# Kernel optimization log

Measured on AMD Instinct MI355X. Metric: run time of the kernel, lower is better.

The kernel has to match this reference:

```python
import jax, jax.numpy as jnp
import numpy as np

N_NODES = 100000
N_EDGES = 1600000
DIM = 128
N_LAYERS = 3
N_GRAPHS = 2048


def setup_inputs() -> dict:
    key = jax.random.key(0)
    ks = jax.random.split(key, 6)
    x = jax.random.normal(ks[0], (N_NODES, DIM), dtype=jnp.float32)
    edge_index = jax.random.randint(ks[1], (2, N_EDGES), 0, N_NODES, dtype=jnp.int64)
    batch = jnp.sort(jax.random.randint(ks[2], (N_NODES,), 0, N_GRAPHS, dtype=jnp.int64))
    scale = 1.0 / np.sqrt(DIM)
    W1 = jax.random.normal(ks[3], (N_LAYERS, DIM, DIM), dtype=jnp.float32) * scale
    b1 = jnp.zeros((N_LAYERS, DIM), dtype=jnp.float32)
    W2 = jax.random.normal(ks[4], (N_LAYERS, DIM, DIM), dtype=jnp.float32) * scale
    b2 = jnp.zeros((N_LAYERS, DIM), dtype=jnp.float32)
    return {"x": x, "edge_index": edge_index, "batch": batch,
            "W1": W1, "b1": b1, "W2": W2, "b2": b2}


def reference(x, edge_index, batch, W1, b1, W2, b2):
    src, dst = edge_index[0], edge_index[1]
    n = x.shape[0]
    n_layers = W1.shape[0]
    for l in range(n_layers):
        # GINConv (eps=0): h_i = MLP( sum_{j in N(i)} x_j + x_i )
        agg = jax.ops.segment_sum(x[src], dst, num_segments=n)  # [N, D]
        h = agg + x
        h = jnp.maximum(h @ W1[l] + b1[l], 0.0) @ W2[l] + b2[l]
        x = jnp.maximum(h, 0.0)  # outer self.act
    # global_mean_pool over graph ids
    sums = jax.ops.segment_sum(x, batch, num_segments=N_GRAPHS)  # [G, D]
    counts = jax.ops.segment_sum(jnp.ones((n,), x.dtype), batch, num_segments=N_GRAPHS)
    return sums / jnp.maximum(counts, 1.0)[:, None]
```

## Files before the change

kernel.cpp:

```cpp
#include <hip/hip_runtime.h>
#include <hip/hip_bf16.h>
#include <stdint.h>

#define N_NODES  100000
#define N_PAD    100032
#define N_EDGES  1600000
#define DIM      128
#define N_LAYERS 3
#define N_GRAPHS 2048

#define BSHIFT   8
#define NBUCKET  391
#define P1CHUNK  4096
#define P1GRID   391

typedef _Float16 f16;
typedef __attribute__((ext_vector_type(4))) _Float16 f16x4;
typedef __attribute__((ext_vector_type(8))) _Float16 f16x8;
typedef __attribute__((ext_vector_type(4))) float f32x4;

#define MFMA16(a, b, c) __builtin_amdgcn_mfma_f32_16x16x32_f16((a), (b), (c), 0, 0, 0)

#define OFF_OFFS  0u
#define OFF_BHT   400064u
#define OFF_GCUR  401664u
#define OFF_BLKH  403264u
#define OFF_ESRC  1014848u
#define OFF_PAIR  7414848u
#define OFF_X16   13814848u
#define OFF_A16   39423040u
#define OFF_B16   65031232u
#define OFF_W1T   90639424u
#define OFF_W2T   90737728u


#define CVTX_BLOCKS 6250
#define CVTW_BLOCKS 384
#define ZERO_BLOCKS 128
#define PRE_GRID    (CVTX_BLOCKS + CVTW_BLOCKS + P1GRID + ZERO_BLOCKS)

__global__ __launch_bounds__(256) void k_pre(
    const float* __restrict__ x, const float* __restrict__ W1, const float* __restrict__ W2,
    f16* __restrict__ x16, f16* __restrict__ W1t, f16* __restrict__ W2t,
    const int* __restrict__ dst, int* __restrict__ btot, int* __restrict__ blkh,
    float* __restrict__ outp)
{
    __shared__ int h[NBUCKET];
    int b = blockIdx.x, tid = threadIdx.x;
    if (b < CVTX_BLOCKS) {
        size_t i = ((size_t)b * 256 + tid) * 8;
        float4 v0 = *(const float4*)&x[i];
        float4 v1 = *(const float4*)&x[i + 4];
        f16x8 o;
        o[0] = (f16)v0.x; o[1] = (f16)v0.y; o[2] = (f16)v0.z; o[3] = (f16)v0.w;
        o[4] = (f16)v1.x; o[5] = (f16)v1.y; o[6] = (f16)v1.z; o[7] = (f16)v1.w;
        *(f16x8*)&x16[i] = o;
    } else if (b < CVTX_BLOCKS + CVTW_BLOCKS) {
        int t = (b - CVTX_BLOCKS) * 256 + tid;
        bool first = t < 49152;
        const float* W = first ? W1 : W2;
        f16* Wt = first ? W1t : W2t;
        int u = first ? t : t - 49152;
        int l = u >> 14;
        int kn = u & 16383;
        int k = kn >> 7, nn = kn & 127;
        Wt[l * 16384 + nn * 128 + k] = (f16)W[u];
    } else if (b < CVTX_BLOCKS + CVTW_BLOCKS + P1GRID) {
        int bb = b - CVTX_BLOCKS - CVTW_BLOCKS;
        for (int i = tid; i < NBUCKET; i += 256) h[i] = 0;
        __syncthreads();
        int base = bb * P1CHUNK;
        int n = min(P1CHUNK, N_EDGES - base);
        for (int i = tid; i < n; i += 256)
            atomicAdd(&h[dst[base + i] >> BSHIFT], 1);
        __syncthreads();
        for (int i = tid; i < NBUCKET; i += 256) {
            blkh[bb * NBUCKET + i] = h[i];
            atomicAdd(&btot[i], h[i]);
        }
    } else {
        int bb = b - CVTX_BLOCKS - CVTW_BLOCKS - P1GRID;
        size_t i = ((size_t)bb * 256 + tid) * 8;
        float4 z = {0.f, 0.f, 0.f, 0.f};
        *(float4*)&outp[i] = z;
        *(float4*)&outp[i + 4] = z;
    }
}


__global__ __launch_bounds__(256) void k_part1(const int* __restrict__ src, const int* __restrict__ dst,
                                               const int* __restrict__ blkh, const int* __restrict__ btot,
                                               int* __restrict__ gcur, uint32_t* __restrict__ pairs) {
    __shared__ int bs[512];
    __shared__ int gbase[NBUCKET];
    __shared__ int cur[NBUCKET];
    int t = threadIdx.x, b = blockIdx.x;
    bs[t]       = (t < NBUCKET) ? btot[t] : 0;
    bs[t + 256] = (t + 256 < NBUCKET) ? btot[t + 256] : 0;
    __syncthreads();
    for (int off = 1; off < 512; off <<= 1) {
        int a0 = (t >= off) ? bs[t - off] : 0;
        int a1 = (t + 256 >= off) ? bs[t + 256 - off] : 0;
        __syncthreads();
        bs[t] += a0; bs[t + 256] += a1;
        __syncthreads();
    }
    for (int i = t; i < NBUCKET; i += 256) {
        int ex = (i == 0) ? 0 : bs[i - 1];
        int h = blkh[b * NBUCKET + i];
        gbase[i] = ex + atomicAdd(&gcur[i], h);
        cur[i] = 0;
    }
    __syncthreads();
    int base = b * P1CHUNK;
    int n = min(P1CHUNK, N_EDGES - base);
    for (int i = t; i < n; i += 256) {
        int d = dst[base + i], s = src[base + i];
        int bin = d >> BSHIFT;
        int slot = atomicAdd(&cur[bin], 1);
        pairs[gbase[bin] + slot] = ((uint32_t)s << 8) | (uint32_t)(d & 255);
    }
}


__global__ __launch_bounds__(256) void k_part2(const uint32_t* __restrict__ pairs,
                                               const int* __restrict__ btot,
                                               int* __restrict__ offs, int* __restrict__ esrc) {
    __shared__ int bs[512];
    __shared__ int cnt[256];
    __shared__ int cur[256];
    __shared__ int sc[256];
    int t = threadIdx.x, b = blockIdx.x;
    bs[t]       = (t < NBUCKET) ? btot[t] : 0;
    bs[t + 256] = (t + 256 < NBUCKET) ? btot[t + 256] : 0;
    __syncthreads();
    for (int off = 1; off < 512; off <<= 1) {
        int a0 = (t >= off) ? bs[t - off] : 0;
        int a1 = (t + 256 >= off) ? bs[t + 256 - off] : 0;
        __syncthreads();
        bs[t] += a0; bs[t + 256] += a1;
        __syncthreads();
    }
    int e0 = (b == 0) ? 0 : bs[b - 1];
    int e1 = bs[b];
    if (b == 0 && t == 0) offs[N_NODES] = N_EDGES;
    int n0 = b << BSHIFT;
    int nn = min(256, N_NODES - n0);
    cnt[t] = 0;
    __syncthreads();
    for (int i = e0 + t; i < e1; i += 256)
        atomicAdd(&cnt[pairs[i] & 255], 1);
    __syncthreads();
    int my = cnt[t];
    sc[t] = my;
    __syncthreads();
    for (int off = 1; off < 256; off <<= 1) {
        int v = (t >= off) ? sc[t - off] : 0;
        __syncthreads();
        sc[t] += v;
        __syncthreads();
    }
    int excl = sc[t] - my;
    cur[t] = excl;
    if (t < nn) offs[n0 + t] = e0 + excl;
    __syncthreads();
    for (int i = e0 + t; i < e1; i += 256) {
        uint32_t p = pairs[i];
        int pos = e0 + atomicAdd(&cur[p & 255], 1);
        esrc[pos] = (int)(p >> 8);
    }
}


#define BM 64
#define LDS_K 136

template <bool POOL>
__global__ __launch_bounds__(512) void k_fused(
    const f16* __restrict__ xin, f16* __restrict__ xout,
    const int* __restrict__ offs, const int* __restrict__ esrc,
    const f16* __restrict__ W1t, const float* __restrict__ b1,
    const f16* __restrict__ W2t, const float* __restrict__ b2,
    const int* __restrict__ batch, float* __restrict__ gsum)
{
    __shared__ __align__(16) f16 tile[BM * LDS_K];
    __shared__ int sbatch[BM];
    __shared__ int wcur;
    int tid  = threadIdx.x;
    int lane = tid & 63;
    int w    = tid >> 6;
    int fr   = lane & 15;
    int fg   = lane >> 4;
    int row0 = blockIdx.x * BM;

    if (tid == 0) wcur = 0;
    if (POOL && tid < BM) {
        int node = row0 + tid;
        sbatch[tid] = (node < N_NODES) ? batch[node] : -1;
    }
    __syncthreads();

    {
        const f16x8* xr = (const f16x8*)xin;
        int c = fr;
        int gl = lane & 48;
        for (;;) {
            int slot;
            if ((lane & 15) == 0) slot = atomicAdd(&wcur, 1);
            slot = __shfl(slot, gl);
            if (slot >= BM) break;
            int node = row0 + slot;
            f16x8 sum = {(f16)0, (f16)0, (f16)0, (f16)0, (f16)0, (f16)0, (f16)0, (f16)0};
            if (node < N_NODES) {
                sum = xr[(size_t)node * 16 + c];
                int e0 = offs[node], e1 = offs[node + 1];
                int e = e0;
                for (; e + 8 <= e1; e += 8) {
                    int s0 = esrc[e + 0], s1 = esrc[e + 1], s2 = esrc[e + 2], s3 = esrc[e + 3];
                    int s4 = esrc[e + 4], s5 = esrc[e + 5], s6 = esrc[e + 6], s7 = esrc[e + 7];
                    f16x8 v0 = xr[(size_t)s0 * 16 + c], v1 = xr[(size_t)s1 * 16 + c];
                    f16x8 v2 = xr[(size_t)s2 * 16 + c], v3 = xr[(size_t)s3 * 16 + c];
                    f16x8 v4 = xr[(size_t)s4 * 16 + c], v5 = xr[(size_t)s5 * 16 + c];
                    f16x8 v6 = xr[(size_t)s6 * 16 + c], v7 = xr[(size_t)s7 * 16 + c];
                    sum += (v0 + v1) + (v2 + v3);
                    sum += (v4 + v5) + (v6 + v7);
                }
                if (e < e1) {
                    int i1 = e + 1, i2 = e + 2, i3 = e + 3, i4 = e + 4, i5 = e + 5, i6 = e + 6, i7 = e + 7;
                    bool k1 = i1 < e1, k2 = i2 < e1, k3 = i3 < e1, k4 = i4 < e1,
                         k5 = i5 < e1, k6 = i6 < e1, k7 = i7 < e1;
                    int s0 = esrc[e];
                    int s1 = esrc[k1 ? i1 : e], s2 = esrc[k2 ? i2 : e], s3 = esrc[k3 ? i3 : e];
                    int s4 = esrc[k4 ? i4 : e], s5 = esrc[k5 ? i5 : e], s6 = esrc[k6 ? i6 : e];
                    int s7 = esrc[k7 ? i7 : e];
                    f16x8 v0 = xr[(size_t)s0 * 16 + c], v1 = xr[(size_t)s1 * 16 + c];
                    f16x8 v2 = xr[(size_t)s2 * 16 + c], v3 = xr[(size_t)s3 * 16 + c];
                    f16x8 v4 = xr[(size_t)s4 * 16 + c], v5 = xr[(size_t)s5 * 16 + c];
                    f16x8 v6 = xr[(size_t)s6 * 16 + c], v7 = xr[(size_t)s7 * 16 + c];
                    sum += v0;
                    if (k1) sum += v1;
                    if (k2) sum += v2;
                    if (k3) sum += v3;
                    if (k4) sum += v4;
                    if (k5) sum += v5;
                    if (k6) sum += v6;
                    if (k7) sum += v7;
                }
            }
            *(f16x8*)&tile[slot * LDS_K + c * 8] = sum;
        }
    }

    int col = w * 16 + fr;
    f16x8 wf[4];
    float4 bv;
#pragma unroll
    for (int ks = 0; ks < 4; ks++)
        wf[ks] = *(const f16x8*)&W1t[col * DIM + ks * 32 + fg * 8];
    bv = *(const float4*)&b1[w * 16 + fg * 4];
    __syncthreads();

    f32x4 acc[4];
#pragma unroll
    for (int mt = 0; mt < 4; mt++) acc[mt] = (f32x4){0.f, 0.f, 0.f, 0.f};
#pragma unroll
    for (int mt = 0; mt < 4; mt++)
#pragma unroll
        for (int ks = 0; ks < 4; ks++) {
            f16x8 a = *(const f16x8*)&tile[(mt * 16 + fr) * LDS_K + ks * 32 + fg * 8];
            acc[mt] = MFMA16(wf[ks], a, acc[mt]);
        }
    __syncthreads();

#pragma unroll
    for (int mt = 0; mt < 4; mt++) {
        f16x4 hv;
        hv[0] = (f16)fmaxf(acc[mt][0] + bv.x, 0.f);
        hv[1] = (f16)fmaxf(acc[mt][1] + bv.y, 0.f);
        hv[2] = (f16)fmaxf(acc[mt][2] + bv.z, 0.f);
        hv[3] = (f16)fmaxf(acc[mt][3] + bv.w, 0.f);
        *(f16x4*)&tile[(mt * 16 + fr) * LDS_K + w * 16 + fg * 4] = hv;
    }

#pragma unroll
    for (int ks = 0; ks < 4; ks++)
        wf[ks] = *(const f16x8*)&W2t[col * DIM + ks * 32 + fg * 8];
    bv = *(const float4*)&b2[w * 16 + fg * 4];
    __syncthreads();

#pragma unroll
    for (int mt = 0; mt < 4; mt++) acc[mt] = (f32x4){0.f, 0.f, 0.f, 0.f};
#pragma unroll
    for (int mt = 0; mt < 4; mt++)
#pragma unroll
        for (int ks = 0; ks < 4; ks++) {
            f16x8 a = *(const f16x8*)&tile[(mt * 16 + fr) * LDS_K + ks * 32 + fg * 8];
            acc[mt] = MFMA16(wf[ks], a, acc[mt]);
        }

    if (!POOL) {
#pragma unroll
        for (int mt = 0; mt < 4; mt++) {
            f16x4 ov;
            ov[0] = (f16)fmaxf(acc[mt][0] + bv.x, 0.f);
            ov[1] = (f16)fmaxf(acc[mt][1] + bv.y, 0.f);
            ov[2] = (f16)fmaxf(acc[mt][2] + bv.z, 0.f);
            ov[3] = (f16)fmaxf(acc[mt][3] + bv.w, 0.f);
            *(f16x4*)&xout[(size_t)(row0 + mt * 16 + fr) * DIM + w * 16 + fg * 4] = ov;
        }
    } else {
        __syncthreads();
#pragma unroll
        for (int mt = 0; mt < 4; mt++) {
            f16x4 ov;
            ov[0] = (f16)fmaxf(acc[mt][0] + bv.x, 0.f);
            ov[1] = (f16)fmaxf(acc[mt][1] + bv.y, 0.f);
            ov[2] = (f16)fmaxf(acc[mt][2] + bv.z, 0.f);
            ov[3] = (f16)fmaxf(acc[mt][3] + bv.w, 0.f);
            *(f16x4*)&tile[(mt * 16 + fr) * LDS_K + w * 16 + fg * 4] = ov;
        }
        __syncthreads();

        int half = tid >> 7;
        int d = tid & 127;
        int rA = half * 16, rB = rA + 16;
        float s = 0.f;
        int curg = sbatch[rA];
        for (int r = rA; r < rB; r++) {
            int g = sbatch[r];
            if (g != curg) {
                if (curg >= 0) atomicAdd(&gsum[(size_t)curg * DIM + d], s);
                s = 0.f; curg = g;
            }
            if (g >= 0) s += (float)tile[r * LDS_K + d];
        }
        if (curg >= 0) atomicAdd(&gsum[(size_t)curg * DIM + d], s);
    }
}


__global__ void k_div(float* __restrict__ out, const int* __restrict__ batch) {
    int g = blockIdx.x;
    int d = threadIdx.x;
    int lo = 0, hi = N_NODES;
    while (lo < hi) { int m = (lo + hi) >> 1; if (batch[m] < g) lo = m + 1; else hi = m; }
    int start = lo;
    hi = N_NODES;
    while (lo < hi) { int m = (lo + hi) >> 1; if (batch[m] <= g) lo = m + 1; else hi = m; }
    int end = lo;
    float cntf = (float)(end - start);
    out[(size_t)g * DIM + d] /= fmaxf(cntf, 1.f);
}


extern "C" void kernel_launch(void* const* d_in, const int* in_sizes, int n_in,
                              void* d_out, int out_size, void* d_ws, size_t ws_size,
                              hipStream_t stream) {
    const float* x     = (const float*)d_in[0];
    const int*   ei    = (const int*)d_in[1];
    const int*   batch = (const int*)d_in[2];
    const float* W1    = (const float*)d_in[3];
    const float* b1    = (const float*)d_in[4];
    const float* W2    = (const float*)d_in[5];
    const float* b2    = (const float*)d_in[6];
    const int* srcp = ei;
    const int* dstp = ei + N_EDGES;

    char* ws = (char*)d_ws;
    int*      offs  = (int*)(ws + OFF_OFFS);
    int*      btot  = (int*)(ws + OFF_BHT);
    int*      gcur  = (int*)(ws + OFF_GCUR);
    int*      blkh  = (int*)(ws + OFF_BLKH);
    int*      esrc  = (int*)(ws + OFF_ESRC);
    uint32_t* pairs = (uint32_t*)(ws + OFF_PAIR);
    f16*      x16   = (f16*)(ws + OFF_X16);
    f16*      a16   = (f16*)(ws + OFF_A16);
    f16*      b16   = (f16*)(ws + OFF_B16);
    f16*      w1t   = (f16*)(ws + OFF_W1T);
    f16*      w2t   = (f16*)(ws + OFF_W2T);
    float*    outp  = (float*)d_out;

    hipMemsetAsync(btot, 0, 3200, stream);
    k_pre<<<PRE_GRID, 256, 0, stream>>>(x, W1, W2, x16, w1t, w2t, dstp, btot, blkh, outp);

    k_part1<<<P1GRID, 256, 0, stream>>>(srcp, dstp, blkh, btot, gcur, pairs);
    k_part2<<<NBUCKET, 256, 0, stream>>>(pairs, btot, offs, esrc);

    k_fused<false><<<N_PAD / BM, 512, 0, stream>>>(x16, a16, offs, esrc,
                                                   w1t, b1, w2t, b2, batch, outp);
    k_fused<false><<<N_PAD / BM, 512, 0, stream>>>(a16, b16, offs, esrc,
                                                   w1t + 16384, b1 + DIM, w2t + 16384, b2 + DIM, batch, outp);
    k_fused<true><<<N_PAD / BM, 512, 0, stream>>>(b16, a16, offs, esrc,
                                                  w1t + 32768, b1 + 2 * DIM, w2t + 32768, b2 + 2 * DIM, batch, outp);

    k_div<<<N_GRAPHS, DIM, 0, stream>>>(outp, batch);
}
```

Baseline: 338.1 us.

## Move conversions into part2 kernel and use static row assignment in aggregation

The bucket histogram now runs alone in the first kernel. The x/W fp16 conversions and the output zeroing move into the same launch as the CSR second pass, so the light histogram and scatter stages run earlier and the bandwidth-heavy conversion overlaps with part2. In the fused GIN kernel, the LDS atomic work-stealing row counter and its barrier are replaced by a fixed mapping of two rows per 16-lane group. This removes atomics and a sync but gives up dynamic load balancing across uneven node degrees.

```diff
diff --git a/kernel.cpp b/kernel.cpp
--- a/kernel.cpp
+++ b/kernel.cpp
@@ -34,56 +34,20 @@
 #define OFF_W2T   90737728u
 
 
-#define CVTX_BLOCKS 6250
-#define CVTW_BLOCKS 384
-#define ZERO_BLOCKS 128
-#define PRE_GRID    (CVTX_BLOCKS + CVTW_BLOCKS + P1GRID + ZERO_BLOCKS)
-
-__global__ __launch_bounds__(256) void k_pre(
-    const float* __restrict__ x, const float* __restrict__ W1, const float* __restrict__ W2,
-    f16* __restrict__ x16, f16* __restrict__ W1t, f16* __restrict__ W2t,
-    const int* __restrict__ dst, int* __restrict__ btot, int* __restrict__ blkh,
-    float* __restrict__ outp)
-{
+__global__ __launch_bounds__(256) void k_bhist(const int* __restrict__ dst,
+                                               int* __restrict__ btot, int* __restrict__ blkh) {
     __shared__ int h[NBUCKET];
-    int b = blockIdx.x, tid = threadIdx.x;
-    if (b < CVTX_BLOCKS) {
-        size_t i = ((size_t)b * 256 + tid) * 8;
-        float4 v0 = *(const float4*)&x[i];
-        float4 v1 = *(const float4*)&x[i + 4];
-        f16x8 o;
-        o[0] = (f16)v0.x; o[1] = (f16)v0.y; o[2] = (f16)v0.z; o[3] = (f16)v0.w;
-        o[4] = (f16)v1.x; o[5] = (f16)v1.y; o[6] = (f16)v1.z; o[7] = (f16)v1.w;
-        *(f16x8*)&x16[i] = o;
-    } else if (b < CVTX_BLOCKS + CVTW_BLOCKS) {
-        int t = (b - CVTX_BLOCKS) * 256 + tid;
-        bool first = t < 49152;
-        const float* W = first ? W1 : W2;
-        f16* Wt = first ? W1t : W2t;
-        int u = first ? t : t - 49152;
-        int l = u >> 14;
-        int kn = u & 16383;
-        int k = kn >> 7, nn = kn & 127;
-        Wt[l * 16384 + nn * 128 + k] = (f16)W[u];
-    } else if (b < CVTX_BLOCKS + CVTW_BLOCKS + P1GRID) {
-        int bb = b - CVTX_BLOCKS - CVTW_BLOCKS;
-        for (int i = tid; i < NBUCKET; i += 256) h[i] = 0;
-        __syncthreads();
-        int base = bb * P1CHUNK;
-        int n = min(P1CHUNK, N_EDGES - base);
-        for (int i = tid; i < n; i += 256)
-            atomicAdd(&h[dst[base + i] >> BSHIFT], 1);
-        __syncthreads();
-        for (int i = tid; i < NBUCKET; i += 256) {
-            blkh[bb * NBUCKET + i] = h[i];
-            atomicAdd(&btot[i], h[i]);
-        }
-    } else {
-        int bb = b - CVTX_BLOCKS - CVTW_BLOCKS - P1GRID;
-        size_t i = ((size_t)bb * 256 + tid) * 8;
-        float4 z = {0.f, 0.f, 0.f, 0.f};
-        *(float4*)&outp[i] = z;
-        *(float4*)&outp[i + 4] = z;
+    int tid = threadIdx.x, b = blockIdx.x;
+    for (int i = tid; i < NBUCKET; i += 256) h[i] = 0;
+    __syncthreads();
+    int base = b * P1CHUNK;
+    int n = min(P1CHUNK, N_EDGES - base);
+    for (int i = tid; i < n; i += 256)
+        atomicAdd(&h[dst[base + i] >> BSHIFT], 1);
+    __syncthreads();
+    for (int i = tid; i < NBUCKET; i += 256) {
+        blkh[b * NBUCKET + i] = h[i];
+        atomicAdd(&btot[i], h[i]);
     }
 }
 
@@ -123,51 +87,89 @@
 }
 
 
-__global__ __launch_bounds__(256) void k_part2(const uint32_t* __restrict__ pairs,
-                                               const int* __restrict__ btot,
-                                               int* __restrict__ offs, int* __restrict__ esrc) {
+#define M_PART2 NBUCKET
+#define M_CVTX  6250
+#define M_CVTW  384
+#define M_ZERO  128
+#define M_GRID  (M_PART2 + M_CVTX + M_CVTW + M_ZERO)
+
+__global__ __launch_bounds__(256) void k_merged(
+    const uint32_t* __restrict__ pairs, const int* __restrict__ btot,
+    int* __restrict__ offs, int* __restrict__ esrc,
+    const float* __restrict__ x, const float* __restrict__ W1, const float* __restrict__ W2,
+    f16* __restrict__ x16, f16* __restrict__ W1t, f16* __restrict__ W2t,
+    float* __restrict__ outp)
+{
     __shared__ int bs[512];
     __shared__ int cnt[256];
     __shared__ int cur[256];
     __shared__ int sc[256];
-    int t = threadIdx.x, b = blockIdx.x;
-    bs[t]       = (t < NBUCKET) ? btot[t] : 0;
-    bs[t + 256] = (t + 256 < NBUCKET) ? btot[t + 256] : 0;
-    __syncthreads();
-    for (int off = 1; off < 512; off <<= 1) {
-        int a0 = (t >= off) ? bs[t - off] : 0;
-        int a1 = (t + 256 >= off) ? bs[t + 256 - off] : 0;
-        __syncthreads();
-        bs[t] += a0; bs[t + 256] += a1;
-        __syncthreads();
-    }
-    int e0 = (b == 0) ? 0 : bs[b - 1];
-    int e1 = bs[b];
-    if (b == 0 && t == 0) offs[N_NODES] = N_EDGES;
-    int n0 = b << BSHIFT;
-    int nn = min(256, N_NODES - n0);
-    cnt[t] = 0;
-    __syncthreads();
-    for (int i = e0 + t; i < e1; i += 256)
-        atomicAdd(&cnt[pairs[i] & 255], 1);
-    __syncthreads();
-    int my = cnt[t];
-    sc[t] = my;
-    __syncthreads();
-    for (int off = 1; off < 256; off <<= 1) {
-        int v = (t >= off) ? sc[t - off] : 0;
-        __syncthreads();
-        sc[t] += v;
-        __syncthreads();
-    }
-    int excl = sc[t] - my;
-    cur[t] = excl;
-    if (t < nn) offs[n0 + t] = e0 + excl;
-    __syncthreads();
-    for (int i = e0 + t; i < e1; i += 256) {
-        uint32_t p = pairs[i];
-        int pos = e0 + atomicAdd(&cur[p & 255], 1);
-        esrc[pos] = (int)(p >> 8);
+    int t = threadIdx.x, blk = blockIdx.x;
+
+    if (blk < M_PART2) {
+        int b = blk;
+        bs[t]       = (t < NBUCKET) ? btot[t] : 0;
+        bs[t + 256] = (t + 256 < NBUCKET) ? btot[t + 256] : 0;
+        __syncthreads();
+        for (int off = 1; off < 512; off <<= 1) {
+            int a0 = (t >= off) ? bs[t - off] : 0;
+            int a1 = (t + 256 >= off) ? bs[t + 256 - off] : 0;
+            __syncthreads();
+            bs[t] += a0; bs[t + 256] += a1;
+            __syncthreads();
+        }
+        int e0 = (b == 0) ? 0 : bs[b - 1];
+        int e1 = bs[b];
+        if (b == 0 && t == 0) offs[N_NODES] = N_EDGES;
+        int n0 = b << BSHIFT;
+        int nn = min(256, N_NODES - n0);
+        cnt[t] = 0;
+        __syncthreads();
+        for (int i = e0 + t; i < e1; i += 256)
+            atomicAdd(&cnt[pairs[i] & 255], 1);
+        __syncthreads();
+        int my = cnt[t];
+        sc[t] = my;
+        __syncthreads();
+        for (int off = 1; off < 256; off <<= 1) {
+            int v = (t >= off) ? sc[t - off] : 0;
+            __syncthreads();
+            sc[t] += v;
+            __syncthreads();
+        }
+        int excl = sc[t] - my;
+        cur[t] = excl;
+        if (t < nn) offs[n0 + t] = e0 + excl;
+        __syncthreads();
+        for (int i = e0 + t; i < e1; i += 256) {
+            uint32_t p = pairs[i];
+            int pos = e0 + atomicAdd(&cur[p & 255], 1);
+            esrc[pos] = (int)(p >> 8);
+        }
+    } else if (blk < M_PART2 + M_CVTX) {
+        size_t i = ((size_t)(blk - M_PART2) * 256 + t) * 8;
+        float4 v0 = *(const float4*)&x[i];
+        float4 v1 = *(const float4*)&x[i + 4];
+        f16x8 o;
+        o[0] = (f16)v0.x; o[1] = (f16)v0.y; o[2] = (f16)v0.z; o[3] = (f16)v0.w;
+        o[4] = (f16)v1.x; o[5] = (f16)v1.y; o[6] = (f16)v1.z; o[7] = (f16)v1.w;
+        *(f16x8*)&x16[i] = o;
+    } else if (blk < M_PART2 + M_CVTX + M_CVTW) {
+        int u = (blk - M_PART2 - M_CVTX) * 256 + t;
+        bool first = u < 49152;
+        const float* W = first ? W1 : W2;
+        f16* Wt = first ? W1t : W2t;
+        int v = first ? u : u - 49152;
+        int l = v >> 14;
+        int kn = v & 16383;
+        int k = kn >> 7, nn = kn & 127;
+        Wt[l * 16384 + nn * 128 + k] = (f16)W[v];
+    } else {
+        int bb = blk - M_PART2 - M_CVTX - M_CVTW;
+        size_t i = ((size_t)bb * 256 + t) * 8;
+        float4 z = {0.f, 0.f, 0.f, 0.f};
+        *(float4*)&outp[i] = z;
+        *(float4*)&outp[i + 4] = z;
     }
 }
 
@@ -185,7 +187,6 @@
 {
     __shared__ __align__(16) f16 tile[BM * LDS_K];
     __shared__ int sbatch[BM];
-    __shared__ int wcur;
     int tid  = threadIdx.x;
     int lane = tid & 63;
     int w    = tid >> 6;
@@ -193,23 +194,18 @@
     int fg   = lane >> 4;
     int row0 = blockIdx.x * BM;
 
-    if (tid == 0) wcur = 0;
     if (POOL && tid < BM) {
         int node = row0 + tid;
         sbatch[tid] = (node < N_NODES) ? batch[node] : -1;
     }
-    __syncthreads();
 
     {
         const f16x8* xr = (const f16x8*)xin;
         int c = fr;
-        int gl = lane & 48;
-        for (;;) {
-            int slot;
-            if ((lane & 15) == 0) slot = atomicAdd(&wcur, 1);
-            slot = __shfl(slot, gl);
-            if (slot >= BM) break;
-            int node = row0 + slot;
+#pragma unroll
+        for (int b_ = 0; b_ < 2; b_++) {
+            int r = w * 8 + b_ * 4 + fg;
+            int node = row0 + r;
             f16x8 sum = {(f16)0, (f16)0, (f16)0, (f16)0, (f16)0, (f16)0, (f16)0, (f16)0};
             if (node < N_NODES) {
                 sum = xr[(size_t)node * 16 + c];
@@ -247,7 +243,7 @@
                     if (k7) sum += v7;
                 }
             }
-            *(f16x8*)&tile[slot * LDS_K + c * 8] = sum;
+            *(f16x8*)&tile[r * LDS_K + c * 8] = sum;
         }
     }
 
@@ -381,10 +377,11 @@
     float*    outp  = (float*)d_out;
 
     hipMemsetAsync(btot, 0, 3200, stream);
-    k_pre<<<PRE_GRID, 256, 0, stream>>>(x, W1, W2, x16, w1t, w2t, dstp, btot, blkh, outp);
-
+
+    k_bhist<<<P1GRID, 256, 0, stream>>>(dstp, btot, blkh);
     k_part1<<<P1GRID, 256, 0, stream>>>(srcp, dstp, blkh, btot, gcur, pairs);
-    k_part2<<<NBUCKET, 256, 0, stream>>>(pairs, btot, offs, esrc);
+    k_merged<<<M_GRID, 256, 0, stream>>>(pairs, btot, offs, esrc,
+                                         x, W1, W2, x16, w1t, w2t, outp);
 
     k_fused<false><<<N_PAD / BM, 512, 0, stream>>>(x16, a16, offs, esrc,
                                                    w1t, b1, w2t, b2, batch, outp);
```

After: 336.5 us. No clear change (-0.5%).
